# Kernel optimization log

Hardware: AMD Instinct MI355X
Metric: run time of the kernel (lower is better)

## Reference

```python
import jax, jax.numpy as jnp
import numpy as np

CUTOFF = 5.0
N_ENV = 8
F0, F1 = 16, 32  # filter_dims
D = 256          # feature_dim


def setup_inputs() -> dict:
    key = jax.random.key(0)
    ks = jax.random.split(key, 12)
    B, E, N = 128, 64, 32
    r = jax.random.normal(ks[0], (B, E, 3), jnp.float32) * 3.0
    # neighbors placed near r so distances fall inside the cutoff
    r_nb = r[..., None, :] + jax.random.normal(ks[1], (B, E, N, 3), jnp.float32) * 1.5
    ee_scales = jax.random.uniform(ks[2], (N_ENV,), jnp.float32, 0.5, CUTOFF)
    ee_kernel = jax.random.normal(ks[3], (4, F0), jnp.float32) / jnp.sqrt(4.0)
    ee_bias = jax.random.normal(ks[4], (F0,), jnp.float32) * 2.0
    beta_kernel = jax.random.normal(ks[5], (F0 + N_ENV, F1), jnp.float32) / jnp.sqrt(F0 + N_ENV + 0.0)
    beta_bias = jnp.zeros((F1,), jnp.float32)
    gamma_kernel = jax.random.normal(ks[6], (F1, D), jnp.float32) / jnp.sqrt(F1 + 0.0)
    dense1_kernel = jax.random.normal(ks[7], (4, D), jnp.float32) / jnp.sqrt(4.0)
    dense1_bias = jnp.zeros((D,), jnp.float32)
    out_kernel = jax.random.normal(ks[8], (D, D), jnp.float32) / jnp.sqrt(D + 0.0)
    out_bias = jnp.zeros((D,), jnp.float32)
    return dict(r=r, r_nb=r_nb, ee_scales=ee_scales, ee_kernel=ee_kernel, ee_bias=ee_bias,
                beta_kernel=beta_kernel, beta_bias=beta_bias, gamma_kernel=gamma_kernel,
                dense1_kernel=dense1_kernel, dense1_bias=dense1_bias,
                out_kernel=out_kernel, out_bias=out_bias)


def reference(r, r_nb, ee_scales, ee_kernel, ee_bias, beta_kernel, beta_bias,
              gamma_kernel, dense1_kernel, dense1_bias, out_kernel, out_bias):
    # pairwise diff features: [dist, dx, dy, dz] per neighbor
    diff = r_nb - r[..., None, :]                       # [B,E,N,3]
    dist = jnp.linalg.norm(diff, axis=-1, keepdims=True)  # [B,E,N,1]
    feats = jnp.concatenate([dist, diff], axis=-1)      # [B,E,N,4]

    # PairwiseFilter (beta_ee): envelopes + small dense, gated by smooth cutoff
    env = jnp.exp(-jnp.square(dist / ee_scales))        # [B,E,N,N_ENV]
    h = jnp.tanh(feats @ ee_kernel + ee_bias)           # [B,E,N,F0]
    x = dist / CUTOFF
    fcut = jnp.where(x < 1.0, 0.5 * (jnp.cos(jnp.pi * x) + 1.0), 0.0)
    beta = (jnp.concatenate([h, env], axis=-1) @ beta_kernel + beta_bias) * fcut  # [B,E,N,F1]

    gamma = beta @ gamma_kernel                         # [B,E,N,D]

    # rescale features: first column (dist) becomes log1p(dist)
    inp = feats / dist * jnp.log1p(dist)                # [B,E,N,4]
    feat = jax.nn.silu(inp @ dense1_kernel + dense1_bias)  # [B,E,N,D]

    res = jnp.einsum('...id,...id->...d', feat, gamma)  # sum over neighbors -> [B,E,D]
    res = jax.nn.silu(res @ out_kernel + out_bias)
    return res
```

## Files before the change

kernel.cpp:

```cpp
#include <hip/hip_runtime.h>
#include <hip/hip_bf16.h>

constexpr int NB   = 32;
constexpr int NENV = 8;
constexpr int F0   = 16;
constexpr int F1   = 32;
constexpr int D    = 256;
constexpr int PAIRS = 128 * 64;
constexpr float CUT = 5.0f;
constexpr int WT_STRIDE = 264;

typedef float f32x4 __attribute__((ext_vector_type(4)));
typedef short s16x8 __attribute__((ext_vector_type(8)));

__device__ __forceinline__ float fast_rcp(float x) { return __builtin_amdgcn_rcpf(x); }
__device__ __forceinline__ float silu(float a) {
  return a * fast_rcp(1.0f + __expf(-a));
}
__device__ __forceinline__ float fast_tanh(float t) {
  return 1.0f - 2.0f * fast_rcp(__expf(2.0f * t) + 1.0f);
}
__device__ __forceinline__ unsigned short f2bf(float f) {
  __hip_bfloat16 h = __float2bfloat16(f);
  unsigned short u; __builtin_memcpy(&u, &h, 2); return u;
}

__global__ __launch_bounds__(256, 4) void moon_phase12(
    const float* __restrict__ r,
    const float* __restrict__ r_nb,
    const float* __restrict__ ee_scales,
    const float* __restrict__ ee_kernel,
    const float* __restrict__ ee_bias,
    const float* __restrict__ beta_kernel,
    const float* __restrict__ beta_bias,
    const float* __restrict__ gamma_kernel,
    const float* __restrict__ dense1_kernel,
    const float* __restrict__ dense1_bias,
    const float* __restrict__ out_kernel,
    unsigned short* __restrict__ resh,
    unsigned short* __restrict__ wt)
{
  __shared__ float s_eek[4 * F0];
  __shared__ float s_eeb[F0];
  __shared__ float s_bk[(F0 + NENV) * F1];
  __shared__ float s_bb[F1];
  __shared__ float s_is2[NENV];
  __shared__ unsigned short s_ghT[4][D * 8];
  __shared__ float s_d1k[4 * D];
  __shared__ float s_d1b[D];
  __shared__ unsigned short s_betah[4][4][NB * 8];
  __shared__ float s_inp[4][NB * 8];

  const int tid = threadIdx.x;
  const int w   = tid >> 6;
  const int l   = tid & 63;
  const int be  = blockIdx.x * 4 + w;

  if (blockIdx.x < 64) {
    const int i  = blockIdx.x * 256 + tid;
    const int d  = i >> 6;
    const int kg = i & 63;
    ushort4 p;
    p.x = f2bf(out_kernel[(4 * kg + 0) * D + d]);
    p.y = f2bf(out_kernel[(4 * kg + 1) * D + d]);
    p.z = f2bf(out_kernel[(4 * kg + 2) * D + d]);
    p.w = f2bf(out_kernel[(4 * kg + 3) * D + d]);
    *(ushort4*)&wt[d * WT_STRIDE + 4 * kg] = p;
  }

  for (int i = tid; i < 888; i += 256) {
    if (i < 64)        s_eek[i]       = ee_kernel[i];
    else if (i < 80)   s_eeb[i - 64]  = ee_bias[i - 64];
    else if (i < 848)  s_bk[i - 80]   = beta_kernel[i - 80];
    else if (i < 880)  s_bb[i - 848]  = beta_bias[i - 848];
    else { float s = ee_scales[i - 880]; s_is2[i - 880] = 1.0f / (s * s); }
  }
  {
    const int d = tid;
    unsigned int pk[16];
    #pragma unroll
    for (int k2 = 0; k2 < 16; ++k2) {
      unsigned short lo = f2bf(gamma_kernel[(2 * k2 + 0) * D + d]);
      unsigned short hi = f2bf(gamma_kernel[(2 * k2 + 1) * D + d]);
      pk[k2] = (unsigned int)lo | ((unsigned int)hi << 16);
    }
    #pragma unroll
    for (int g = 0; g < 4; ++g)
      *(uint4*)&s_ghT[g][d * 8] = make_uint4(pk[4*g], pk[4*g+1], pk[4*g+2], pk[4*g+3]);
  }
  *(float4*)&s_d1k[4 * tid] = *(const float4*)(dense1_kernel + 4 * tid);
  if (tid < 64) *(float4*)&s_d1b[4 * tid] = *(const float4*)(dense1_bias + 4 * tid);

  __syncthreads();

  {
    const int n  = l & 31;
    const int cg = l >> 5;
    float rx = r[be * 3 + 0];
    float ry = r[be * 3 + 1];
    float rz = r[be * 3 + 2];
    const float* rn = r_nb + (be * NB + n) * 3;
    float dx = rn[0] - rx;
    float dy = rn[1] - ry;
    float dz = rn[2] - rz;
    float d2 = dx * dx + dy * dy + dz * dz;
    float dist = sqrtf(d2);
    float feats[4] = {dist, dx, dy, dz};
    float h[F0];
    #pragma unroll
    for (int j = 0; j < F0; ++j) {
      float t = s_eeb[j];
      #pragma unroll
      for (int i = 0; i < 4; ++i) t += feats[i] * s_eek[i * F0 + j];
      h[j] = fast_tanh(t);
    }
    float env[NENV];
    #pragma unroll
    for (int s = 0; s < NENV; ++s) env[s] = __expf(-d2 * s_is2[s]);
    float xc = dist * (1.0f / CUT);
    float fcut = (xc < 1.0f)
               ? 0.5f * (__cosf(3.14159265358979323846f * xc) + 1.0f)
               : 0.0f;
    if (cg == 0) {
      float lp = log1pf(dist);
      float inv = lp / dist;
      *(float4*)&s_inp[w][n * 8] = make_float4(lp, dx * inv, dy * inv, dz * inv);
    }
    unsigned int pk[8];
    #pragma unroll
    for (int c4 = 0; c4 < 4; ++c4) {
      float bb[4];
      #pragma unroll
      for (int cc = 0; cc < 4; ++cc) {
        int c = cg * 16 + c4 * 4 + cc;
        float a = s_bb[c];
        #pragma unroll
        for (int k = 0; k < F0; ++k) a += h[k] * s_bk[k * F1 + c];
        #pragma unroll
        for (int s = 0; s < NENV; ++s) a += env[s] * s_bk[(F0 + s) * F1 + c];
        bb[cc] = a * fcut;
      }
      pk[c4 * 2 + 0] = (unsigned int)f2bf(bb[0]) | ((unsigned int)f2bf(bb[1]) << 16);
      pk[c4 * 2 + 1] = (unsigned int)f2bf(bb[2]) | ((unsigned int)f2bf(bb[3]) << 16);
    }
    *(uint4*)&s_betah[w][2 * cg + 0][n * 8] = make_uint4(pk[0], pk[1], pk[2], pk[3]);
    *(uint4*)&s_betah[w][2 * cg + 1][n * 8] = make_uint4(pk[4], pk[5], pk[6], pk[7]);
  }
  __syncthreads();

  const int li = l & 15;
  const int g  = l >> 4;

  s16x8 a0 = *(const s16x8*)&s_betah[w][g][(0 * 16 + li) * 8];
  s16x8 a1 = *(const s16x8*)&s_betah[w][g][(1 * 16 + li) * 8];

  float4 ip[8];
  #pragma unroll
  for (int mt = 0; mt < 2; ++mt)
    #pragma unroll
    for (int reg = 0; reg < 4; ++reg)
      ip[mt * 4 + reg] = *(const float4*)&s_inp[w][(mt * 16 + g * 4 + reg) * 8];

  float rpart[16];
  #pragma unroll
  for (int nt = 0; nt < 16; ++nt) {
    const int d = nt * 16 + li;
    s16x8 b = *(const s16x8*)&s_ghT[g][d * 8];
    f32x4 z = {0.f, 0.f, 0.f, 0.f};
    f32x4 c0 = __builtin_amdgcn_mfma_f32_16x16x32_bf16(a0, b, z, 0, 0, 0);
    f32x4 c1 = __builtin_amdgcn_mfma_f32_16x16x32_bf16(a1, b, z, 0, 0, 0);
    float w0 = s_d1k[0 * D + d];
    float w1 = s_d1k[1 * D + d];
    float w2 = s_d1k[2 * D + d];
    float w3 = s_d1k[3 * D + d];
    float bia = s_d1b[d];
    float p = 0.f;
    #pragma unroll
    for (int reg = 0; reg < 4; ++reg) {
      float4 i0 = ip[reg];
      float aa0 = bia + i0.x * w0 + i0.y * w1 + i0.z * w2 + i0.w * w3;
      p += silu(aa0) * c0[reg];
      float4 i1 = ip[4 + reg];
      float aa1 = bia + i1.x * w0 + i1.y * w1 + i1.z * w2 + i1.w * w3;
      p += silu(aa1) * c1[reg];
    }
    rpart[nt] = p;
  }
  #pragma unroll
  for (int nt = 0; nt < 16; ++nt) {
    float v = rpart[nt];
    v += __shfl_xor(v, 16);
    v += __shfl_xor(v, 32);
    rpart[nt] = v;
  }
  float* s_resw = &s_inp[w][0];
  #pragma unroll
  for (int nt = 0; nt < 16; ++nt) {
    if (g == (nt & 3)) s_resw[nt * 16 + li] = rpart[nt];
  }
  float4 rv = *(const float4*)&s_resw[4 * l];
  ushort4 rp;
  rp.x = f2bf(rv.x); rp.y = f2bf(rv.y); rp.z = f2bf(rv.z); rp.w = f2bf(rv.w);
  *(ushort4*)(resh + be * D + 4 * l) = rp;
}

__global__ __launch_bounds__(256, 4) void moon_outgemm(
    const unsigned short* __restrict__ resh,
    const unsigned short* __restrict__ wt,
    const float* __restrict__ bias,
    float* __restrict__ out)
{
  const int tid = threadIdx.x;
  const int w   = tid >> 6;
  const int l   = tid & 63;
  const int li  = l & 15;
  const int g   = l >> 4;
  const int row0 = blockIdx.x * 16;

  float bi[4];
  #pragma unroll
  for (int nt = 0; nt < 4; ++nt) bi[nt] = bias[(w * 4 + nt) * 16 + li];

  f32x4 acc[4] = {{0.f,0.f,0.f,0.f},{0.f,0.f,0.f,0.f},{0.f,0.f,0.f,0.f},{0.f,0.f,0.f,0.f}};
  const unsigned short* ap = resh + (row0 + li) * D + g * 8;
  const unsigned short* bp = wt + (w * 64 + li) * WT_STRIDE + g * 8;

  #pragma unroll
  for (int ks = 0; ks < 8; ++ks) {
    s16x8 a = *(const s16x8*)(ap + ks * 32);
    #pragma unroll
    for (int nt = 0; nt < 4; ++nt) {
      s16x8 b = *(const s16x8*)(bp + nt * 16 * WT_STRIDE + ks * 32);
      acc[nt] = __builtin_amdgcn_mfma_f32_16x16x32_bf16(a, b, acc[nt], 0, 0, 0);
    }
  }
  #pragma unroll
  for (int nt = 0; nt < 4; ++nt) {
    #pragma unroll
    for (int reg = 0; reg < 4; ++reg) {
      int row = row0 + g * 4 + reg;
      int col = (w * 4 + nt) * 16 + li;
      out[row * D + col] = silu(acc[nt][reg] + bi[nt]);
    }
  }
}

extern "C" void kernel_launch(void* const* d_in, const int* in_sizes, int n_in,
                              void* d_out, int out_size, void* d_ws, size_t ws_size,
                              hipStream_t stream) {
  const float* r            = (const float*)d_in[0];
  const float* r_nb         = (const float*)d_in[1];
  const float* ee_scales    = (const float*)d_in[2];
  const float* ee_kernel    = (const float*)d_in[3];
  const float* ee_bias      = (const float*)d_in[4];
  const float* beta_kernel  = (const float*)d_in[5];
  const float* beta_bias    = (const float*)d_in[6];
  const float* gamma_kernel = (const float*)d_in[7];
  const float* dense1_kernel= (const float*)d_in[8];
  const float* dense1_bias  = (const float*)d_in[9];
  const float* out_kernel   = (const float*)d_in[10];
  const float* out_bias     = (const float*)d_in[11];
  float* out = (float*)d_out;

  unsigned short* resh = (unsigned short*)d_ws;
  unsigned short* wt   = (unsigned short*)((char*)d_ws + 4 * 1024 * 1024);

  hipLaunchKernelGGL(moon_phase12, dim3(PAIRS / 4), dim3(256), 0, stream,
                     r, r_nb, ee_scales, ee_kernel, ee_bias,
                     beta_kernel, beta_bias, gamma_kernel,
                     dense1_kernel, dense1_bias, out_kernel, resh, wt);
  hipLaunchKernelGGL(moon_outgemm, dim3(PAIRS / 16), dim3(256), 0, stream,
                     resh, wt, out_bias, out);
}
```

Before: 128.2 us.

## Compute dense1 features with bf16 MFMA and split output GEMM across column halves

The per-neighbor dense1 projection (4 inputs plus bias to 256 outputs), previously done with scalar FMAs from fp32 shared memory, now runs as an extra pair of bf16 MFMAs. The inputs are padded to k=8 with a constant 1 column that carries the bias, and only lanes in group 0 supply nonzero operands. Separately, the output GEMM kernel now covers half the columns per block and launches twice as many blocks to raise parallelism. This cuts VALU work and shared memory use but adds bf16 rounding to the dense1 inputs, weights and bias.

```diff
diff --git a/kernel.cpp b/kernel.cpp
--- a/kernel.cpp
+++ b/kernel.cpp
@@ -46,15 +46,17 @@
   __shared__ float s_bb[F1];
   __shared__ float s_is2[NENV];
   __shared__ unsigned short s_ghT[4][D * 8];
-  __shared__ float s_d1k[4 * D];
-  __shared__ float s_d1b[D];
+  __shared__ unsigned short s_d1kT[D * 8];
   __shared__ unsigned short s_betah[4][4][NB * 8];
-  __shared__ float s_inp[4][NB * 8];
+  __shared__ float4 s_scratch[4][64];
 
   const int tid = threadIdx.x;
   const int w   = tid >> 6;
   const int l   = tid & 63;
   const int be  = blockIdx.x * 4 + w;
+
+  unsigned short* s_inph = (unsigned short*)&s_scratch[w][0];
+  float*          s_resw = (float*)&s_scratch[w][0];
 
   if (blockIdx.x < 64) {
     const int i  = blockIdx.x * 256 + tid;
@@ -88,8 +90,15 @@
     for (int g = 0; g < 4; ++g)
       *(uint4*)&s_ghT[g][d * 8] = make_uint4(pk[4*g], pk[4*g+1], pk[4*g+2], pk[4*g+3]);
   }
-  *(float4*)&s_d1k[4 * tid] = *(const float4*)(dense1_kernel + 4 * tid);
-  if (tid < 64) *(float4*)&s_d1b[4 * tid] = *(const float4*)(dense1_bias + 4 * tid);
+  {
+    const int d = tid;
+    unsigned int p0 = (unsigned int)f2bf(dense1_kernel[0 * D + d])
+                    | ((unsigned int)f2bf(dense1_kernel[1 * D + d]) << 16);
+    unsigned int p1 = (unsigned int)f2bf(dense1_kernel[2 * D + d])
+                    | ((unsigned int)f2bf(dense1_kernel[3 * D + d]) << 16);
+    unsigned int p2 = (unsigned int)f2bf(dense1_bias[d]);
+    *(uint4*)&s_d1kT[d * 8] = make_uint4(p0, p1, p2, 0u);
+  }
 
   __syncthreads();
 
@@ -124,7 +133,9 @@
     if (cg == 0) {
       float lp = log1pf(dist);
       float inv = lp / dist;
-      *(float4*)&s_inp[w][n * 8] = make_float4(lp, dx * inv, dy * inv, dz * inv);
+      unsigned int q0 = (unsigned int)f2bf(lp) | ((unsigned int)f2bf(dx * inv) << 16);
+      unsigned int q1 = (unsigned int)f2bf(dy * inv) | ((unsigned int)f2bf(dz * inv) << 16);
+      *(uint4*)&s_inph[n * 8] = make_uint4(q0, q1, 0x3F80u , 0u);
     }
     unsigned int pk[8];
     #pragma unroll
@@ -154,35 +165,30 @@
   s16x8 a0 = *(const s16x8*)&s_betah[w][g][(0 * 16 + li) * 8];
   s16x8 a1 = *(const s16x8*)&s_betah[w][g][(1 * 16 + li) * 8];
 
-  float4 ip[8];
-  #pragma unroll
-  for (int mt = 0; mt < 2; ++mt)
-    #pragma unroll
-    for (int reg = 0; reg < 4; ++reg)
-      ip[mt * 4 + reg] = *(const float4*)&s_inp[w][(mt * 16 + g * 4 + reg) * 8];
+  s16x8 zi = {0, 0, 0, 0, 0, 0, 0, 0};
+  s16x8 ai0 = zi, ai1 = zi;
+  if (g == 0) {
+    ai0 = *(const s16x8*)&s_inph[(0 * 16 + li) * 8];
+    ai1 = *(const s16x8*)&s_inph[(1 * 16 + li) * 8];
+  }
 
   float rpart[16];
   #pragma unroll
   for (int nt = 0; nt < 16; ++nt) {
     const int d = nt * 16 + li;
     s16x8 b = *(const s16x8*)&s_ghT[g][d * 8];
+    s16x8 bd = zi;
+    if (g == 0) bd = *(const s16x8*)&s_d1kT[d * 8];
     f32x4 z = {0.f, 0.f, 0.f, 0.f};
     f32x4 c0 = __builtin_amdgcn_mfma_f32_16x16x32_bf16(a0, b, z, 0, 0, 0);
     f32x4 c1 = __builtin_amdgcn_mfma_f32_16x16x32_bf16(a1, b, z, 0, 0, 0);
-    float w0 = s_d1k[0 * D + d];
-    float w1 = s_d1k[1 * D + d];
-    float w2 = s_d1k[2 * D + d];
-    float w3 = s_d1k[3 * D + d];
-    float bia = s_d1b[d];
+    f32x4 f0 = __builtin_amdgcn_mfma_f32_16x16x32_bf16(ai0, bd, z, 0, 0, 0);
+    f32x4 f1 = __builtin_amdgcn_mfma_f32_16x16x32_bf16(ai1, bd, z, 0, 0, 0);
     float p = 0.f;
     #pragma unroll
     for (int reg = 0; reg < 4; ++reg) {
-      float4 i0 = ip[reg];
-      float aa0 = bia + i0.x * w0 + i0.y * w1 + i0.z * w2 + i0.w * w3;
-      p += silu(aa0) * c0[reg];
-      float4 i1 = ip[4 + reg];
-      float aa1 = bia + i1.x * w0 + i1.y * w1 + i1.z * w2 + i1.w * w3;
-      p += silu(aa1) * c1[reg];
+      p += silu(f0[reg]) * c0[reg];
+      p += silu(f1[reg]) * c1[reg];
     }
     rpart[nt] = p;
   }
@@ -193,7 +199,6 @@
     v += __shfl_xor(v, 32);
     rpart[nt] = v;
   }
-  float* s_resw = &s_inp[w][0];
   #pragma unroll
   for (int nt = 0; nt < 16; ++nt) {
     if (g == (nt & 3)) s_resw[nt * 16 + li] = rpart[nt];
@@ -210,36 +215,39 @@
     const float* __restrict__ bias,
     float* __restrict__ out)
 {
-  const int tid = threadIdx.x;
-  const int w   = tid >> 6;
-  const int l   = tid & 63;
-  const int li  = l & 15;
-  const int g   = l >> 4;
-  const int row0 = blockIdx.x * 16;
-
-  float bi[4];
-  #pragma unroll
-  for (int nt = 0; nt < 4; ++nt) bi[nt] = bias[(w * 4 + nt) * 16 + li];
-
-  f32x4 acc[4] = {{0.f,0.f,0.f,0.f},{0.f,0.f,0.f,0.f},{0.f,0.f,0.f,0.f},{0.f,0.f,0.f,0.f}};
+  const int tid  = threadIdx.x;
+  const int w    = tid >> 6;
+  const int l    = tid & 63;
+  const int li   = l & 15;
+  const int g    = l >> 4;
+  const int tile = blockIdx.x >> 1;
+  const int half = blockIdx.x & 1;
+  const int row0 = tile * 16;
+  const int col0 = half * 128 + w * 32;
+
+  float bi[2];
+  #pragma unroll
+  for (int nt = 0; nt < 2; ++nt) bi[nt] = bias[col0 + nt * 16 + li];
+
+  f32x4 acc[2] = {{0.f,0.f,0.f,0.f},{0.f,0.f,0.f,0.f}};
   const unsigned short* ap = resh + (row0 + li) * D + g * 8;
-  const unsigned short* bp = wt + (w * 64 + li) * WT_STRIDE + g * 8;
+  const unsigned short* bp = wt + (col0 + li) * WT_STRIDE + g * 8;
 
   #pragma unroll
   for (int ks = 0; ks < 8; ++ks) {
     s16x8 a = *(const s16x8*)(ap + ks * 32);
     #pragma unroll
-    for (int nt = 0; nt < 4; ++nt) {
+    for (int nt = 0; nt < 2; ++nt) {
       s16x8 b = *(const s16x8*)(bp + nt * 16 * WT_STRIDE + ks * 32);
       acc[nt] = __builtin_amdgcn_mfma_f32_16x16x32_bf16(a, b, acc[nt], 0, 0, 0);
     }
   }
   #pragma unroll
-  for (int nt = 0; nt < 4; ++nt) {
+  for (int nt = 0; nt < 2; ++nt) {
     #pragma unroll
     for (int reg = 0; reg < 4; ++reg) {
       int row = row0 + g * 4 + reg;
-      int col = (w * 4 + nt) * 16 + li;
+      int col = col0 + nt * 16 + li;
       out[row * D + col] = silu(acc[nt][reg] + bi[nt]);
     }
   }
@@ -269,6 +277,6 @@
                      r, r_nb, ee_scales, ee_kernel, ee_bias,
                      beta_kernel, beta_bias, gamma_kernel,
                      dense1_kernel, dense1_bias, out_kernel, resh, wt);
-  hipLaunchKernelGGL(moon_outgemm, dim3(PAIRS / 16), dim3(256), 0, stream,
+  hipLaunchKernelGGL(moon_outgemm, dim3(PAIRS / 16 * 2), dim3(256), 0, stream,
                      resh, wt, out_bias, out);
 }
```

New measurement: 195.2 us. 1.52x slower.
